# Optimization experiments

Hardware: AMD Instinct MI355X
Metric: run time of the kernel (lower is better)

Reference implementation:

```python
import jax, jax.numpy as jnp
import numpy as np

K = 9        # kernel_size
DIL = 6      # dilation
SIGMA = 1.0  # gaussian bandwidth
BN_EPS = 1e-5


def setup_inputs() -> dict:
    key = jax.random.key(0)
    ks = jax.random.split(key, 6)
    B, Cin, Cout, N = 8, 256, 256, 8192
    x = jax.random.normal(ks[0], (B, Cin, N), jnp.float32)
    coords = jax.random.normal(ks[1], (B, 3, N), jnp.float32)
    rotations = jax.random.normal(ks[2], (B, 3, N), jnp.float32)
    distances = jax.random.uniform(ks[3], (B, N), jnp.float32)
    W = jax.random.normal(ks[4], (Cout, Cin, K), jnp.float32) * 0.02
    bias = jnp.zeros((Cout,), jnp.float32)
    gamma = jnp.ones((Cout,), jnp.float32)
    beta = jnp.zeros((Cout,), jnp.float32)
    return dict(x=x, coords=coords, rotations=rotations, distances=distances,
                W=W, bias=bias, gamma=gamma, beta=beta)


def _tap_weight(c0, cj, r0, rj, d0, dj, sigma):
    # Gaussian weight from 3D coordinate offset + curve-distance offset,
    # modulated by rotation alignment |cos(r_i, r_j)|.
    dc = jnp.sum((c0 - cj) ** 2, axis=1)          # [B,N]
    dd = (d0 - dj) ** 2                            # [B,N]
    g = jnp.exp(-(dc + dd) / (2.0 * sigma * sigma))
    num = jnp.sum(r0 * rj, axis=1)
    den = jnp.sqrt(jnp.sum(r0 * r0, axis=1) * jnp.sum(rj * rj, axis=1)) + 1e-8
    return g * jnp.abs(num / den)                  # [B,N]


def reference(x, coords, rotations, distances, W, bias, gamma, beta):
    B, Cin, N = x.shape
    Cout = W.shape[0]
    pad = DIL * (K // 2)  # same-length output for the dilated conv
    pw3 = ((0, 0), (0, 0), (pad, pad))
    xp = jnp.pad(x, pw3)
    cp = jnp.pad(coords, pw3)
    rp = jnp.pad(rotations, pw3)
    dp = jnp.pad(distances, ((0, 0), (pad, pad)))

    out = jnp.zeros((B, Cout, N), x.dtype)
    for k in range(K):  # fixed, small tap loop
        off = k * DIL
        xk = jax.lax.dynamic_slice_in_dim(xp, off, N, axis=2)
        ck = jax.lax.dynamic_slice_in_dim(cp, off, N, axis=2)
        rk = jax.lax.dynamic_slice_in_dim(rp, off, N, axis=2)
        dk = jax.lax.dynamic_slice_in_dim(dp, off, N, axis=1)
        g = _tap_weight(coords, ck, rotations, rk, distances, dk, SIGMA)  # [B,N]
        out = out + jnp.einsum('oc,bcn->bon', W[:, :, k], xk * g[:, None, :])
    out = out + bias[None, :, None]

    # BatchNorm1d (training-mode batch stats over B and N per channel)
    mean = jnp.mean(out, axis=(0, 2), keepdims=True)
    var = jnp.var(out, axis=(0, 2), keepdims=True)
    out = (out - mean) / jnp.sqrt(var + BN_EPS)
    out = out * gamma[None, :, None] + beta[None, :, None]
    return jax.nn.relu(out)
```

## Files before the change

### kernel.cpp

```cpp
#include <hip/hip_runtime.h>

#define KTAPS 9
#define DIL 6
#define BN_EPS 1e-5f
#define BB 8
#define CIN 256
#define COUT 256
#define NPTS 8192
#define BN 128
#define NCHUNK 72

typedef __attribute__((ext_vector_type(8))) short short8;
typedef __attribute__((ext_vector_type(4))) float f32x4;

__device__ __forceinline__ unsigned short f2bf(float f) {
  union { float f; unsigned u; } v; v.f = f;
  unsigned r = v.u + 0x7fffu + ((v.u >> 16) & 1u);
  return (unsigned short)(r >> 16);
}

__device__ __forceinline__ void async16(const void* gp, void* lp) {
  __builtin_amdgcn_global_load_lds(
      (const __attribute__((address_space(1))) unsigned int*)gp,
      (__attribute__((address_space(3))) unsigned int*)lp, 16, 0, 0);
}

__global__ __launch_bounds__(256)
void pre_kernel(const float* __restrict__ coords, const float* __restrict__ rot,
                const float* __restrict__ dist, const float* __restrict__ W,
                float* __restrict__ g, short* __restrict__ Wa,
                float* __restrict__ sums) {
  int bid = blockIdx.x;
  if (bid < 2304) {
    int gid = bid * 256 + threadIdx.x;
    int n = gid & (NPTS - 1);
    int bk = gid >> 13;
    int k = bk % KTAPS;
    int b = bk / KTAPS;
    const float* cb = coords + (size_t)b * 3 * NPTS;
    const float* rb = rot + (size_t)b * 3 * NPTS;
    const float* db = dist + (size_t)b * NPTS;
    int j = n + (k - KTAPS / 2) * DIL;
    float gv = 0.f;
    if (j >= 0 && j < NPTS) {
      float c0x = cb[n], c0y = cb[NPTS + n], c0z = cb[2 * NPTS + n];
      float r0x = rb[n], r0y = rb[NPTS + n], r0z = rb[2 * NPTS + n];
      float dcx = c0x - cb[j], dcy = c0y - cb[NPTS + j], dcz = c0z - cb[2 * NPTS + j];
      float dc = dcx * dcx + dcy * dcy + dcz * dcz;
      float dd = db[n] - db[j];
      dd *= dd;
      float gauss = expf(-(dc + dd) * 0.5f);
      float rjx = rb[j], rjy = rb[NPTS + j], rjz = rb[2 * NPTS + j];
      float num = r0x * rjx + r0y * rjy + r0z * rjz;
      float r0n = r0x * r0x + r0y * r0y + r0z * r0z;
      float den = sqrtf(r0n * (rjx * rjx + rjy * rjy + rjz * rjz)) + 1e-8f;
      gv = gauss * fabsf(num / den);
    }
    g[gid] = gv;
  } else if (bid < 4608) {
    int idx = (bid - 2304) * 256 + threadIdx.x;
    int kk = idx & 31;
    int mi = (idx >> 5) & 255;
    int chunk = idx >> 13;
    int ktap = chunk >> 3;
    int c = ((chunk & 7) << 5) + kk;
    Wa[idx] = (short)f2bf(W[(size_t)mi * (CIN * KTAPS) + c * KTAPS + ktap]);
  } else {
    if (threadIdx.x < 512) sums[threadIdx.x] = 0.f;
  }
}

__global__ __launch_bounds__(256, 2)
void conv_mfma(const float* __restrict__ x, const float* __restrict__ g,
               const short* __restrict__ Wa, const float* __restrict__ bias,
               float* __restrict__ out,
               float* __restrict__ sums1, float* __restrict__ sums2) {
  __shared__ short A_lds[2][256 * 32];
  __shared__ short B_lds[2][BN * 40];

  const int tid = threadIdx.x;
  const int b = blockIdx.y;
  const int n0 = blockIdx.x * BN;
  const int wave = tid >> 6;
  const int lane = tid & 63;
  const int col = lane & 15;
  const int quad = lane >> 4;

  const int sn = tid & 127;
  const int skg = (tid >> 7) * 16;
  const float* xb = x + (size_t)b * CIN * NPTS;
  const float* gb = g + ((size_t)b * KTAPS) * NPTS + n0 + sn;

  f32x4 acc[4][8];
#pragma unroll
  for (int i = 0; i < 4; ++i)
#pragma unroll
    for (int j = 0; j < 8; ++j) acc[i][j] = (f32x4)0.f;

  float xv[16];
  float gval;

  {
    const short* wsrc = Wa + tid * 8;
#pragma unroll
    for (int t = 0; t < 4; ++t)
      async16(wsrc + t * 2048, &A_lds[0][tid * 8 + t * 2048]);
    const int jn = n0 + sn + (0 - 4) * DIL;
    const bool inr = (jn >= 0) && (jn < NPTS);
    const float* xcol = xb + (size_t)skg * NPTS + jn;
    gval = gb[0];
#pragma unroll
    for (int jj = 0; jj < 16; ++jj)
      xv[jj] = inr ? xcol[(size_t)jj * NPTS] : 0.f;
    short8 p0, p1;
#pragma unroll
    for (int jj = 0; jj < 8; ++jj) { p0[jj] = (short)f2bf(xv[jj] * gval); p1[jj] = (short)f2bf(xv[8 + jj] * gval); }
    *(short8*)&B_lds[0][sn * 40 + skg] = p0;
    *(short8*)&B_lds[0][sn * 40 + skg + 8] = p1;
  }
  __syncthreads();

  for (int i = 0; i < NCHUNK; ++i) {
    const int cur = i & 1;
    const int nxt = cur ^ 1;
    const bool more = (i + 1) < NCHUNK;

    if (more) {
      const int i1 = i + 1;
      const short* wsrc = Wa + (size_t)i1 * 8192 + tid * 8;
#pragma unroll
      for (int t = 0; t < 4; ++t)
        async16(wsrc + t * 2048, &A_lds[nxt][tid * 8 + t * 2048]);
      const int k1 = i1 >> 3;
      const int c81 = i1 & 7;
      const int jn = n0 + sn + (k1 - 4) * DIL;
      const bool inr = (jn >= 0) && (jn < NPTS);
      const float* xcol = xb + (size_t)(c81 * 32 + skg) * NPTS + jn;
      gval = gb[(size_t)k1 * NPTS];
#pragma unroll
      for (int jj = 0; jj < 16; ++jj)
        xv[jj] = inr ? xcol[(size_t)jj * NPTS] : 0.f;
    }

    {
      short8 af[4];
#pragma unroll
      for (int m = 0; m < 4; ++m)
        af[m] = *(short8*)&A_lds[cur][(wave * 64 + m * 16 + col) * 32 + quad * 8];
#pragma unroll
      for (int j = 0; j < 8; ++j) {
        short8 bfv = *(short8*)&B_lds[cur][(j * 16 + col) * 40 + quad * 8];
#pragma unroll
        for (int m = 0; m < 4; ++m)
          acc[m][j] = __builtin_amdgcn_mfma_f32_16x16x32_bf16(af[m], bfv, acc[m][j], 0, 0, 0);
      }
    }

    if (more) {
      short8 p0, p1;
#pragma unroll
      for (int jj = 0; jj < 8; ++jj) { p0[jj] = (short)f2bf(xv[jj] * gval); p1[jj] = (short)f2bf(xv[8 + jj] * gval); }
      *(short8*)&B_lds[nxt][sn * 40 + skg] = p0;
      *(short8*)&B_lds[nxt][sn * 40 + skg + 8] = p1;
    }
    __syncthreads();
  }

  const int obase = wave * 64;
  float* outp = out + (size_t)b * COUT * NPTS + n0;
#pragma unroll
  for (int m = 0; m < 4; ++m) {
    const int o0 = obase + m * 16 + quad * 4;
    const float4 bv = *(const float4*)&bias[o0];
#pragma unroll
    for (int j = 0; j < 8; ++j) {
      acc[m][j][0] += bv.x; acc[m][j][1] += bv.y;
      acc[m][j][2] += bv.z; acc[m][j][3] += bv.w;
    }
#pragma unroll
    for (int r = 0; r < 4; ++r) {
      float s1 = 0.f, s2 = 0.f;
#pragma unroll
      for (int j = 0; j < 8; ++j) {
        float v = acc[m][j][r];
        s1 += v; s2 += v * v;
      }
      s1 += __shfl_xor(s1, 1); s2 += __shfl_xor(s2, 1);
      s1 += __shfl_xor(s1, 2); s2 += __shfl_xor(s2, 2);
      s1 += __shfl_xor(s1, 4); s2 += __shfl_xor(s2, 4);
      s1 += __shfl_xor(s1, 8); s2 += __shfl_xor(s2, 8);
      if (col == 0) {
        atomicAdd(&sums1[o0 + r], s1);
        atomicAdd(&sums2[o0 + r], s2);
      }
#pragma unroll
      for (int j = 0; j < 8; ++j)
        outp[(size_t)(o0 + r) * NPTS + j * 16 + col] = acc[m][j][r];
    }
  }
}

__global__ __launch_bounds__(256)
void bn_apply(float* __restrict__ out, const float* __restrict__ sums1,
              const float* __restrict__ sums2, const float* __restrict__ gamma,
              const float* __restrict__ beta) {
  int bo = blockIdx.x;
  int o = bo & (COUT - 1);
  const float inv = 1.f / (float)(BB * NPTS);
  float mean = sums1[o] * inv;
  float var = sums2[o] * inv - mean * mean;
  float scale = gamma[o] * rsqrtf(var + BN_EPS);
  float shift = beta[o] - mean * scale;
  float4* p = (float4*)(out + (size_t)bo * NPTS);
  for (int i = threadIdx.x; i < NPTS / 4; i += blockDim.x) {
    float4 v = p[i];
    v.x = fmaxf(fmaf(v.x, scale, shift), 0.f);
    v.y = fmaxf(fmaf(v.y, scale, shift), 0.f);
    v.z = fmaxf(fmaf(v.z, scale, shift), 0.f);
    v.w = fmaxf(fmaf(v.w, scale, shift), 0.f);
    p[i] = v;
  }
}

extern "C" void kernel_launch(void* const* d_in, const int* in_sizes, int n_in,
                              void* d_out, int out_size, void* d_ws, size_t ws_size,
                              hipStream_t stream) {
  const float* x      = (const float*)d_in[0];
  const float* coords = (const float*)d_in[1];
  const float* rot    = (const float*)d_in[2];
  const float* dist   = (const float*)d_in[3];
  const float* W      = (const float*)d_in[4];
  const float* bias   = (const float*)d_in[5];
  const float* gamma  = (const float*)d_in[6];
  const float* beta   = (const float*)d_in[7];
  float* out = (float*)d_out;

  float* ws    = (float*)d_ws;
  float* sums1 = ws;
  float* sums2 = ws + 256;
  float* g     = ws + 512;
  short* Wa    = (short*)(g + (size_t)BB * KTAPS * NPTS);

  pre_kernel<<<4609, 256, 0, stream>>>(coords, rot, dist, W, g, Wa, sums1);
  conv_mfma<<<dim3(NPTS / BN, BB), 256, 0, stream>>>(x, g, Wa, bias, out, sums1, sums2);
  bn_apply<<<BB * COUT, 256, 0, stream>>>(out, sums1, sums2, gamma, beta);
}
```

Baseline: 292.9 us.

## Fuse tap-weight computation into conv kernel and load weights directly to registers

Removes the precomputed g buffer: each conv block now computes its 9x128 Gaussian tap weights into shared memory at startup, so the g array is never written to and re-read from global memory. Weight fragments are read straight from global into double-buffered registers instead of being staged through LDS with async loads, which frees the A tile's LDS. The x staging is reorganised so each thread loads float2 pairs across 8 channels, the block index interleaves batches, and the main loop is unrolled by 2. Register pressure rises and every block re-reads the weights from global/L2 with no LDS reuse, which is the main risk.

```diff
diff --git a/kernel.cpp b/kernel.cpp
--- a/kernel.cpp
+++ b/kernel.cpp
@@ -9,6 +9,7 @@
 #define NPTS 8192
 #define BN 128
 #define NCHUNK 72
+#define BSTRIDE 40
 
 typedef __attribute__((ext_vector_type(8))) short short8;
 typedef __attribute__((ext_vector_type(4))) float f32x4;
@@ -19,46 +20,12 @@
   return (unsigned short)(r >> 16);
 }
 
-__device__ __forceinline__ void async16(const void* gp, void* lp) {
-  __builtin_amdgcn_global_load_lds(
-      (const __attribute__((address_space(1))) unsigned int*)gp,
-      (__attribute__((address_space(3))) unsigned int*)lp, 16, 0, 0);
-}
-
 __global__ __launch_bounds__(256)
-void pre_kernel(const float* __restrict__ coords, const float* __restrict__ rot,
-                const float* __restrict__ dist, const float* __restrict__ W,
-                float* __restrict__ g, short* __restrict__ Wa,
+void pre_kernel(const float* __restrict__ W, short* __restrict__ Wa,
                 float* __restrict__ sums) {
   int bid = blockIdx.x;
   if (bid < 2304) {
-    int gid = bid * 256 + threadIdx.x;
-    int n = gid & (NPTS - 1);
-    int bk = gid >> 13;
-    int k = bk % KTAPS;
-    int b = bk / KTAPS;
-    const float* cb = coords + (size_t)b * 3 * NPTS;
-    const float* rb = rot + (size_t)b * 3 * NPTS;
-    const float* db = dist + (size_t)b * NPTS;
-    int j = n + (k - KTAPS / 2) * DIL;
-    float gv = 0.f;
-    if (j >= 0 && j < NPTS) {
-      float c0x = cb[n], c0y = cb[NPTS + n], c0z = cb[2 * NPTS + n];
-      float r0x = rb[n], r0y = rb[NPTS + n], r0z = rb[2 * NPTS + n];
-      float dcx = c0x - cb[j], dcy = c0y - cb[NPTS + j], dcz = c0z - cb[2 * NPTS + j];
-      float dc = dcx * dcx + dcy * dcy + dcz * dcz;
-      float dd = db[n] - db[j];
-      dd *= dd;
-      float gauss = expf(-(dc + dd) * 0.5f);
-      float rjx = rb[j], rjy = rb[NPTS + j], rjz = rb[2 * NPTS + j];
-      float num = r0x * rjx + r0y * rjy + r0z * rjz;
-      float r0n = r0x * r0x + r0y * r0y + r0z * r0z;
-      float den = sqrtf(r0n * (rjx * rjx + rjy * rjy + rjz * rjz)) + 1e-8f;
-      gv = gauss * fabsf(num / den);
-    }
-    g[gid] = gv;
-  } else if (bid < 4608) {
-    int idx = (bid - 2304) * 256 + threadIdx.x;
+    int idx = bid * 256 + threadIdx.x;
     int kk = idx & 31;
     int mi = (idx >> 5) & 255;
     int chunk = idx >> 13;
@@ -71,55 +38,94 @@
 }
 
 __global__ __launch_bounds__(256, 2)
-void conv_mfma(const float* __restrict__ x, const float* __restrict__ g,
+void conv_mfma(const float* __restrict__ x, const float* __restrict__ coords,
+               const float* __restrict__ rot, const float* __restrict__ dist,
                const short* __restrict__ Wa, const float* __restrict__ bias,
                float* __restrict__ out,
                float* __restrict__ sums1, float* __restrict__ sums2) {
-  __shared__ short A_lds[2][256 * 32];
-  __shared__ short B_lds[2][BN * 40];
+  __shared__ short B_lds[2][BN * BSTRIDE];
+  __shared__ float g_lds[KTAPS * BN];
 
   const int tid = threadIdx.x;
-  const int b = blockIdx.y;
-  const int n0 = blockIdx.x * BN;
+  const int b = blockIdx.x & 7;
+  const int tile = blockIdx.x >> 3;
+  const int n0 = tile * BN;
+
   const int wave = tid >> 6;
   const int lane = tid & 63;
   const int col = lane & 15;
   const int quad = lane >> 4;
 
-  const int sn = tid & 127;
-  const int skg = (tid >> 7) * 16;
+  {
+    const float* cb = coords + (size_t)b * 3 * NPTS;
+    const float* rb = rot + (size_t)b * 3 * NPTS;
+    const float* db = dist + (size_t)b * NPTS;
+    for (int t = tid; t < KTAPS * BN; t += 256) {
+      int k = t >> 7;
+      int n = n0 + (t & 127);
+      int j = n + (k - KTAPS / 2) * DIL;
+      float gv = 0.f;
+      if (j >= 0 && j < NPTS) {
+        float c0x = cb[n], c0y = cb[NPTS + n], c0z = cb[2 * NPTS + n];
+        float r0x = rb[n], r0y = rb[NPTS + n], r0z = rb[2 * NPTS + n];
+        float dcx = c0x - cb[j], dcy = c0y - cb[NPTS + j], dcz = c0z - cb[2 * NPTS + j];
+        float dc = dcx * dcx + dcy * dcy + dcz * dcz;
+        float dd = db[n] - db[j];
+        dd *= dd;
+        float gauss = expf(-(dc + dd) * 0.5f);
+        float rjx = rb[j], rjy = rb[NPTS + j], rjz = rb[2 * NPTS + j];
+        float num = r0x * rjx + r0y * rjy + r0z * rjz;
+        float r0n = r0x * r0x + r0y * r0y + r0z * r0z;
+        float den = sqrtf(r0n * (rjx * rjx + rjy * rjy + rjz * rjz)) + 1e-8f;
+        gv = gauss * fabsf(num / den);
+      }
+      g_lds[t] = gv;
+    }
+  }
+
+  const int tl = tid & 63;
+  const int tkk = (tid >> 6) * 8;
   const float* xb = x + (size_t)b * CIN * NPTS;
-  const float* gb = g + ((size_t)b * KTAPS) * NPTS + n0 + sn;
+  const short* pA = Wa + ((size_t)(wave * 64 + col) * 32 + quad * 8);
+
+  __syncthreads();
+
+  short8 af[2][4];
+  float2 xv[8];
+  float2 gv;
+
+  {
+    int jn = n0 + 2 * tl - 24;
+    bool valid = (jn >= 0) && (jn < NPTS);
+    int jnc = valid ? jn : (jn < 0 ? 0 : NPTS - 2);
+    const float* px = xb + (size_t)tkk * NPTS + jnc;
+#pragma unroll
+    for (int cc = 0; cc < 8; ++cc) {
+      float2 v = *(const float2*)&px[(size_t)cc * NPTS];
+      xv[cc] = valid ? v : make_float2(0.f, 0.f);
+    }
+#pragma unroll
+    for (int m = 0; m < 4; ++m)
+      af[0][m] = *(const short8*)&pA[m * 512];
+    gv = *(const float2*)&g_lds[2 * tl];
+    short8 p0, p1;
+#pragma unroll
+    for (int cc = 0; cc < 8; ++cc) {
+      p0[cc] = (short)f2bf(xv[cc].x * gv.x);
+      p1[cc] = (short)f2bf(xv[cc].y * gv.y);
+    }
+    *(short8*)&B_lds[0][(2 * tl) * BSTRIDE + tkk] = p0;
+    *(short8*)&B_lds[0][(2 * tl + 1) * BSTRIDE + tkk] = p1;
+  }
+  __syncthreads();
 
   f32x4 acc[4][8];
 #pragma unroll
-  for (int i = 0; i < 4; ++i)
-#pragma unroll
-    for (int j = 0; j < 8; ++j) acc[i][j] = (f32x4)0.f;
-
-  float xv[16];
-  float gval;
-
-  {
-    const short* wsrc = Wa + tid * 8;
-#pragma unroll
-    for (int t = 0; t < 4; ++t)
-      async16(wsrc + t * 2048, &A_lds[0][tid * 8 + t * 2048]);
-    const int jn = n0 + sn + (0 - 4) * DIL;
-    const bool inr = (jn >= 0) && (jn < NPTS);
-    const float* xcol = xb + (size_t)skg * NPTS + jn;
-    gval = gb[0];
-#pragma unroll
-    for (int jj = 0; jj < 16; ++jj)
-      xv[jj] = inr ? xcol[(size_t)jj * NPTS] : 0.f;
-    short8 p0, p1;
-#pragma unroll
-    for (int jj = 0; jj < 8; ++jj) { p0[jj] = (short)f2bf(xv[jj] * gval); p1[jj] = (short)f2bf(xv[8 + jj] * gval); }
-    *(short8*)&B_lds[0][sn * 40 + skg] = p0;
-    *(short8*)&B_lds[0][sn * 40 + skg + 8] = p1;
-  }
-  __syncthreads();
-
+  for (int m = 0; m < 4; ++m)
+#pragma unroll
+    for (int j = 0; j < 8; ++j) acc[m][j] = (f32x4)0.f;
+
+#pragma unroll 2
   for (int i = 0; i < NCHUNK; ++i) {
     const int cur = i & 1;
     const int nxt = cur ^ 1;
@@ -127,41 +133,41 @@
 
     if (more) {
       const int i1 = i + 1;
-      const short* wsrc = Wa + (size_t)i1 * 8192 + tid * 8;
-#pragma unroll
-      for (int t = 0; t < 4; ++t)
-        async16(wsrc + t * 2048, &A_lds[nxt][tid * 8 + t * 2048]);
       const int k1 = i1 >> 3;
       const int c81 = i1 & 7;
-      const int jn = n0 + sn + (k1 - 4) * DIL;
-      const bool inr = (jn >= 0) && (jn < NPTS);
-      const float* xcol = xb + (size_t)(c81 * 32 + skg) * NPTS + jn;
-      gval = gb[(size_t)k1 * NPTS];
-#pragma unroll
-      for (int jj = 0; jj < 16; ++jj)
-        xv[jj] = inr ? xcol[(size_t)jj * NPTS] : 0.f;
-    }
-
-    {
-      short8 af[4];
+      int jn = n0 + 2 * tl + (k1 - 4) * DIL;
+      bool valid = (jn >= 0) && (jn < NPTS);
+      int jnc = valid ? jn : (jn < 0 ? 0 : NPTS - 2);
+      const float* px = xb + (size_t)(c81 * 32 + tkk) * NPTS + jnc;
+#pragma unroll
+      for (int cc = 0; cc < 8; ++cc) {
+        float2 v = *(const float2*)&px[(size_t)cc * NPTS];
+        xv[cc] = valid ? v : make_float2(0.f, 0.f);
+      }
+      const short* pAi = pA + (size_t)i1 * 8192;
 #pragma unroll
       for (int m = 0; m < 4; ++m)
-        af[m] = *(short8*)&A_lds[cur][(wave * 64 + m * 16 + col) * 32 + quad * 8];
-#pragma unroll
-      for (int j = 0; j < 8; ++j) {
-        short8 bfv = *(short8*)&B_lds[cur][(j * 16 + col) * 40 + quad * 8];
-#pragma unroll
-        for (int m = 0; m < 4; ++m)
-          acc[m][j] = __builtin_amdgcn_mfma_f32_16x16x32_bf16(af[m], bfv, acc[m][j], 0, 0, 0);
-      }
+        af[nxt][m] = *(const short8*)&pAi[m * 512];
+      gv = *(const float2*)&g_lds[k1 * BN + 2 * tl];
+    }
+
+#pragma unroll
+    for (int j = 0; j < 8; ++j) {
+      short8 bfv = *(short8*)&B_lds[cur][(j * 16 + col) * BSTRIDE + quad * 8];
+#pragma unroll
+      for (int m = 0; m < 4; ++m)
+        acc[m][j] = __builtin_amdgcn_mfma_f32_16x16x32_bf16(af[cur][m], bfv, acc[m][j], 0, 0, 0);
     }
 
     if (more) {
       short8 p0, p1;
 #pragma unroll
-      for (int jj = 0; jj < 8; ++jj) { p0[jj] = (short)f2bf(xv[jj] * gval); p1[jj] = (short)f2bf(xv[8 + jj] * gval); }
-      *(short8*)&B_lds[nxt][sn * 40 + skg] = p0;
-      *(short8*)&B_lds[nxt][sn * 40 + skg + 8] = p1;
+      for (int cc = 0; cc < 8; ++cc) {
+        p0[cc] = (short)f2bf(xv[cc].x * gv.x);
+        p1[cc] = (short)f2bf(xv[cc].y * gv.y);
+      }
+      *(short8*)&B_lds[nxt][(2 * tl) * BSTRIDE + tkk] = p0;
+      *(short8*)&B_lds[nxt][(2 * tl + 1) * BSTRIDE + tkk] = p1;
     }
     __syncthreads();
   }
@@ -238,10 +244,9 @@
   float* ws    = (float*)d_ws;
   float* sums1 = ws;
   float* sums2 = ws + 256;
-  float* g     = ws + 512;
-  short* Wa    = (short*)(g + (size_t)BB * KTAPS * NPTS);
-
-  pre_kernel<<<4609, 256, 0, stream>>>(coords, rot, dist, W, g, Wa, sums1);
-  conv_mfma<<<dim3(NPTS / BN, BB), 256, 0, stream>>>(x, g, Wa, bias, out, sums1, sums2);
+  short* Wa    = (short*)(ws + 512);
+
+  pre_kernel<<<2305, 256, 0, stream>>>(W, Wa, sums1);
+  conv_mfma<<<512, 256, 0, stream>>>(x, coords, rot, dist, Wa, bias, out, sums1, sums2);
   bn_apply<<<BB * COUT, 256, 0, stream>>>(out, sums1, sums2, gamma, beta);
 }
```

New measurement: 394.2 us. 34.6% more time.
